# Kernel optimization log

Hardware: AMD Instinct MI355X
Metric: run time of the kernel (lower is better)

Reference implementation:

```python
import jax, jax.numpy as jnp
import numpy as np

B_, L_, DM = 8, 1024, 256
DS, DC, EX = 16, 4, 2
DI = EX * DM            # d_inner = 512
DTR = max(1, DM // 16)  # dt_rank = 16


def setup_inputs() -> dict:
    key = jax.random.key(0)
    ks = iter(jax.random.split(key, 40))
    def n(shape, s=0.02):
        return jax.random.normal(next(ks), shape, jnp.float32) * s
    inp = {"x": jax.random.normal(next(ks), (B_, L_, DM), jnp.float32)}
    inp["norm_g"] = jnp.ones((DM,), jnp.float32)
    inp["norm_b"] = jnp.zeros((DM,), jnp.float32)
    for m in ("f", "b"):
        inp[f"inW_{m}"] = n((DM, 2 * DI))
        inp[f"convW_{m}"] = n((DI, DC))
        inp[f"convB_{m}"] = jnp.zeros((DI,), jnp.float32)
        inp[f"xW_{m}"] = n((DI, DTR + 2 * DS))
        inp[f"dtW_{m}"] = n((DTR, DI))
        inp[f"dtB_{m}"] = jnp.zeros((DI,), jnp.float32)
        # ALog init: log of [1..dState] repeated over dInner rows
        inp[f"ALog_{m}"] = jnp.log(jnp.tile(jnp.arange(1, DS + 1, dtype=jnp.float32), (DI, 1)))
        inp[f"Dp_{m}"] = jnp.ones((DI,), jnp.float32)
        inp[f"outW_{m}"] = n((DI, DM))
    inp["fusW"] = n((2 * DM, DM))
    inp["fusB"] = jnp.zeros((DM,), jnp.float32)
    return inp


def _dw_conv(x, w, b):
    # causal depthwise conv1d: x [B,L,DI], w [DI,DC] -> [B,L,DI]
    xc = jnp.transpose(x, (0, 2, 1))  # B,DI,L
    out = jax.lax.conv_general_dilated(
        xc, w[:, None, :], window_strides=(1,), padding=[(DC - 1, 0)],
        dimension_numbers=("NCH", "OIH", "NCH"), feature_group_count=DI)
    return jnp.transpose(out + b[:, None], (0, 2, 1))


def _ssm(x, xW, dtW, dtB, ALog, Dp):
    # x: [B,L,DI]
    A = -jnp.exp(ALog)                                   # [DI,DS]
    xdbl = x @ xW                                        # [B,L,DTR+2*DS]
    dlt, Bp, Cp = jnp.split(xdbl, [DTR, DTR + DS], axis=-1)
    delta = jax.nn.softplus(dlt @ dtW + dtB)             # [B,L,DI]
    dA = jnp.exp(delta[..., None] * A)                   # [B,L,DI,DS]
    dBx = (delta * x)[..., None] * Bp[:, :, None, :]     # [B,L,DI,DS]

    def step(h, t):
        a, bb, c = t
        h = a * h + bb                                   # [B,DI,DS]
        y = jnp.einsum('bdn,bn->bd', h, c)
        return h, y

    h0 = jnp.zeros((x.shape[0], DI, DS), x.dtype)
    _, ys = jax.lax.scan(step, h0, (jnp.moveaxis(dA, 1, 0),
                                    jnp.moveaxis(dBx, 1, 0),
                                    jnp.moveaxis(Cp, 1, 0)))
    return jnp.moveaxis(ys, 0, 1) + Dp * x               # [B,L,DI]


def _mamba(x, inW, convW, convB, xW, dtW, dtB, ALog, Dp, outW):
    xr = x @ inW                                         # [B,L,2*DI]
    xs, res = jnp.split(xr, 2, axis=-1)
    xs = jax.nn.silu(_dw_conv(xs, convW, convB))
    y = _ssm(xs, xW, dtW, dtB, ALog, Dp)
    return (y * jax.nn.silu(res)) @ outW                 # [B,L,DM]


def reference(x, norm_g, norm_b,
              inW_f, convW_f, convB_f, xW_f, dtW_f, dtB_f, ALog_f, Dp_f, outW_f,
              inW_b, convW_b, convB_b, xW_b, dtW_b, dtB_b, ALog_b, Dp_b, outW_b,
              fusW, fusB):
    # LayerNorm
    mu = x.mean(-1, keepdims=True)
    var = ((x - mu) ** 2).mean(-1, keepdims=True)
    xn = (x - mu) * jax.lax.rsqrt(var + 1e-5) * norm_g + norm_b
    # forward-direction Mamba
    xf = _mamba(xn, inW_f, convW_f, convB_f, xW_f, dtW_f, dtB_f, ALog_f, Dp_f, outW_f)
    # backward-direction Mamba (flip along time)
    xb = _mamba(jnp.flip(xn, 1), inW_b, convW_b, convB_b, xW_b, dtW_b, dtB_b, ALog_b, Dp_b, outW_b)
    xb = jnp.flip(xb, 1)
    fused = jnp.concatenate([xf, xb], axis=-1) @ fusW + fusB
    return x + fused  # dropout is identity in eval
```

## Files before the change

kernel.cpp:

```cpp
#include <hip/hip_runtime.h>
#include <cmath>

typedef __bf16 bf16x8 __attribute__((ext_vector_type(8)));
typedef __bf16 bf16x4 __attribute__((ext_vector_type(4)));
typedef float  f32x4  __attribute__((ext_vector_type(4)));
typedef float  f32x2  __attribute__((ext_vector_type(2)));

#define B_  8
#define L_  1024
#define DM  256
#define DI  512
#define DS  16
#define DTR 16
#define M_  (B_*L_)
#define NC  32
#define CT  32
#define CC  64
#define CTC 16

__device__ inline float softplus_f(float z){
  return (z > 20.f) ? z : __logf(1.f + __expf(z));
}
__device__ inline float silu_f(float z){
  return z / (1.f + __expf(-z));
}

__device__ inline int flag_from_x(const void* x){
  const unsigned short* u = (const unsigned short*)x;
  int lane = threadIdx.x & 63;
  unsigned short v = u[2*lane];
  int e = (v >> 7) & 0xFF;
  unsigned long long m = __ballot(e >= 160 || e < 96);
  return __popcll(m) > 16;
}

struct PrepJob { const void* src; void* dst; int rows; int cols; int f32out; };
struct PrepArgs { PrepJob j[26]; int nj; };
struct TJob { const void* src; __bf16* dst; int R; int C; };
struct TArgs { TJob j[3]; int ntiles[3]; int nj; int ntot; };

__global__ __launch_bounds__(256) void wprep_k(TArgs ta, PrepArgs a, const void* xsrc){
  const int f = flag_from_x(xsrc);
  const int tid = threadIdx.x;
  if ((int)blockIdx.x < ta.ntot){
    __shared__ float tile[64][65];
    int bid = blockIdx.x;
    int jj = 0;
    while (jj < ta.nj-1 && bid >= ta.ntiles[jj]) { bid -= ta.ntiles[jj]; jj++; }
    const TJob J = ta.j[jj];
    const int tpr = J.C >> 6;
    const int tr = bid / tpr, tc = bid - tr*tpr;
    const int r0 = tr*64, c0 = tc*64;
    #pragma unroll
    for (int i=0;i<16;i++){
      int idx = i*256 + tid;
      int r = idx >> 6, c = idx & 63;
      long off = (long)(r0+r)*J.C + c0 + c;
      tile[r][c] = f ? ((const float*)J.src)[off] : (float)((const __bf16*)J.src)[off];
    }
    __syncthreads();
    #pragma unroll
    for (int i=0;i<16;i++){
      int idx = i*256 + tid;
      int c = idx >> 6, r = idx & 63;
      J.dst[(long)(c0+c)*J.R + r0 + r] = (__bf16)tile[r][c];
    }
  } else {
    int e = (blockIdx.x - ta.ntot)*256 + tid;
    #pragma unroll 1
    for (int jj=0; jj<a.nj; jj++){
      int sz = a.j[jj].rows * a.j[jj].cols;
      if (e < sz){
        int cols = a.j[jj].cols;
        int r = e / cols, c = e - r*cols;
        float v = f ? ((const float*)a.j[jj].src)[e] : (float)((const __bf16*)a.j[jj].src)[e];
        if (a.j[jj].f32out) ((float*)a.j[jj].dst)[c*a.j[jj].rows + r] = v;
        else ((__bf16*)a.j[jj].dst)[(long)c*a.j[jj].rows + r] = (__bf16)v;
        return;
      }
      e -= sz;
    }
  }
}

__global__ __launch_bounds__(256) void lnw_k(
    const void* x, const __bf16* g, const __bf16* bb, __bf16* xn,
    const __bf16* fusWt, const __bf16* outWr0, const __bf16* outWr1,
    __bf16* BtC0, __bf16* BtC1)
{
  const int bx = blockIdx.x;
  const int tid = threadIdx.x;
  const int lane = tid & 63;
  const int wid = tid >> 6;

  if (bx < M_/4){
    const int f = flag_from_x(x);
    long row = (long)bx*4 + wid;
    long base = row*DM + lane*4;
    float v0,v1,v2,v3;
    if (f){ f32x4 xv = *(const f32x4*)((const float*)x + base);
            v0=xv[0]; v1=xv[1]; v2=xv[2]; v3=xv[3]; }
    else  { bf16x4 xv = *(const bf16x4*)((const __bf16*)x + base);
            v0=(float)xv[0]; v1=(float)xv[1]; v2=(float)xv[2]; v3=(float)xv[3]; }
    float s = v0+v1+v2+v3;
    float q = v0*v0+v1*v1+v2*v2+v3*v3;
    #pragma unroll
    for (int off=32; off>0; off>>=1){ s += __shfl_xor(s,off); q += __shfl_xor(q,off); }
    float mu = s*(1.f/DM), var = q*(1.f/DM)-mu*mu;
    float rs = rsqrtf(var+1e-5f);
    bf16x4 gv = *(const bf16x4*)(g + lane*4);
    bf16x4 bv = *(const bf16x4*)(bb + lane*4);
    bf16x4 o;
    o[0]=(__bf16)((v0-mu)*rs*(float)gv[0]+(float)bv[0]);
    o[1]=(__bf16)((v1-mu)*rs*(float)gv[1]+(float)bv[1]);
    o[2]=(__bf16)((v2-mu)*rs*(float)gv[2]+(float)bv[2]);
    o[3]=(__bf16)((v3-mu)*rs*(float)gv[3]+(float)bv[3]);
    *(bf16x4*)(xn + base) = o;
  } else {
    int b2 = bx - M_/4;
    int wz  = b2 >> 5;
    int rem = b2 & 31;
    int gx = rem & 3, gy = rem >> 2;
    const __bf16* A  = fusWt + wz*DM;
    const __bf16* Bt = wz ? outWr1 : outWr0;
    __bf16* C = wz ? BtC1 : BtC0;
    const int mBase = (gx*4 + wid)*16;
    const int nBase = gy*64;
    const int lm = lane & 15;
    const int kq = (lane >> 4)*8;
    long aoff = (long)(mBase+lm)*(2*DM) + kq;
    long boff[4];
    #pragma unroll
    for (int j=0;j<4;j++) boff[j] = (long)(nBase+j*16+lm)*DM + kq;
    f32x4 acc[4] = {};
    #pragma unroll
    for (int k0=0;k0<DM;k0+=32){
      bf16x8 af = *(const bf16x8*)(A + aoff + k0);
      bf16x8 bfr[4];
      #pragma unroll
      for (int j=0;j<4;j++) bfr[j] = *(const bf16x8*)(Bt + boff[j] + k0);
      #pragma unroll
      for (int j=0;j<4;j++)
        acc[j] = __builtin_amdgcn_mfma_f32_16x16x32_bf16(af, bfr[j], acc[j], 0,0,0);
    }
    #pragma unroll
    for (int rr=0;rr<4;rr++){
      int r = mBase + (lane>>4)*4 + rr;
      #pragma unroll
      for (int j=0;j<4;j++){
        int c = nBase + j*16 + lm;
        C[(long)r*DI + c] = (__bf16)acc[j][rr];
      }
    }
  }
}

template<int BM,int BN,int KK>
__global__ __launch_bounds__(256) void gemm_in_k(
    const __bf16* A, const __bf16* B0, const __bf16* B1,
    __bf16* xz0, __bf16* xz1, __bf16* res0, __bf16* res1,
    int lda, int ldb)
{
  constexpr int TM = BM/2, TN = BN/2;
  constexpr int WMT = TM/16, WNT = TN/16;
  constexpr int LA = BM/64, LB = BN/64;

  const int dir = blockIdx.z;
  const __bf16* Bt = dir ? B1 : B0;
  __bf16* xz  = dir ? xz1 : xz0;
  __bf16* res = dir ? res1 : res0;
  const int tid  = threadIdx.x;
  const int lane = tid & 63;
  const int wid  = tid >> 6;
  const int wm = wid & 1;
  const int wn = wid >> 1;
  const int mBase = blockIdx.x * BM;
  const int nBase = blockIdx.y * BN;
  const int lm = lane & 15;
  const int kq = (lane >> 4) * 8;

  __shared__ __bf16 As[BM*32];
  __shared__ __bf16 Bs[BN*32];

  const __bf16* aS[LA];
  const __bf16* bS[LB];
  {
    int colk = (tid & 3) * 8;
    #pragma unroll
    for (int ld=0; ld<LA; ld++){
      int r = mBase + ld*64 + (tid >> 2);
      if (dir==1){ int b = r >> 10, t = r & (L_-1); r = (b<<10) + (L_-1-t); }
      aS[ld] = A + (long)r*lda + colk;
    }
    #pragma unroll
    for (int ld=0; ld<LB; ld++){
      int r = nBase + ld*64 + (tid >> 2);
      bS[ld] = Bt + (long)r*ldb + colk;
    }
  }

  f32x4 acc[WMT][WNT] = {};
  for (int k0=0; k0<KK; k0+=32){
    #pragma unroll
    for (int ld=0; ld<LA; ld++)
      __builtin_amdgcn_global_load_lds(
        (const __attribute__((address_space(1))) void*)(aS[ld] + k0),
        (__attribute__((address_space(3))) void*)(&As[ld*2048 + tid*8]), 16, 0, 0);
    #pragma unroll
    for (int ld=0; ld<LB; ld++)
      __builtin_amdgcn_global_load_lds(
        (const __attribute__((address_space(1))) void*)(bS[ld] + k0),
        (__attribute__((address_space(3))) void*)(&Bs[ld*2048 + tid*8]), 16, 0, 0);
    __syncthreads();
    bf16x8 af[WMT], bfr[WNT];
    #pragma unroll
    for (int i=0;i<WMT;i++) af[i]  = *(const bf16x8*)&As[(wm*TM + i*16 + lm)*32 + kq];
    #pragma unroll
    for (int j=0;j<WNT;j++) bfr[j] = *(const bf16x8*)&Bs[(wn*TN + j*16 + lm)*32 + kq];
    #pragma unroll
    for (int i=0;i<WMT;i++)
      #pragma unroll
      for (int j=0;j<WNT;j++)
        acc[i][j] = __builtin_amdgcn_mfma_f32_16x16x32_bf16(af[i], bfr[j], acc[i][j], 0,0,0);
    __syncthreads();
  }

  #pragma unroll
  for (int i=0;i<WMT;i++){
    #pragma unroll
    for (int rr=0;rr<4;rr++){
      int r = mBase + wm*TM + i*16 + (lane>>4)*4 + rr;
      #pragma unroll
      for (int j=0;j<WNT;j++){
        int c = nBase + wn*TN + j*16 + lm;
        float v = acc[i][j][rr];
        if (c < DI) xz[(long)r*DI + c] = (__bf16)v;
        else        res[(long)r*DI + (c-DI)] = (__bf16)v;
      }
    }
  }
}

template<int BM,int BN,int KK>
__global__ __launch_bounds__(256) void gemm_fin_k(
    const __bf16* Af, const __bf16* Ab,
    const __bf16* Bt0, const __bf16* Bt1,
    void* Cout, const __bf16* bias, const void* resid)
{
  constexpr int TM = BM/2, TN = BN/2;
  constexpr int WMT = TM/16, WNT = TN/16;
  constexpr int LA = BM/64, LB = BN/64;

  const int of = flag_from_x(resid);
  const int tid  = threadIdx.x;
  const int lane = tid & 63;
  const int wid  = tid >> 6;
  const int wm = wid & 1;
  const int wn = wid >> 1;
  const int mBase = blockIdx.x * BM;
  const int nBase = blockIdx.y * BN;
  const int lm = lane & 15;
  const int kq = (lane >> 4) * 8;

  __shared__ __bf16 As[BM*32];
  __shared__ __bf16 Bs[BN*32];

  f32x4 acc[WMT][WNT] = {};
  #pragma unroll 1
  for (int dd=0; dd<2; dd++){
    const __bf16* A  = dd ? Ab  : Af;
    const __bf16* Bt = dd ? Bt1 : Bt0;
    const __bf16* aS[LA];
    const __bf16* bS[LB];
    {
      int colk = (tid & 3) * 8;
      #pragma unroll
      for (int ld=0; ld<LA; ld++){
        int r = mBase + ld*64 + (tid >> 2);
        if (dd==1){ int b = r >> 10, t = r & (L_-1); r = (b<<10) + (L_-1-t); }
        aS[ld] = A + (long)r*DI + colk;
      }
      #pragma unroll
      for (int ld=0; ld<LB; ld++){
        int r = nBase + ld*64 + (tid >> 2);
        bS[ld] = Bt + (long)r*DI + colk;
      }
    }
    for (int k0=0; k0<KK; k0+=32){
      #pragma unroll
      for (int ld=0; ld<LA; ld++)
        __builtin_amdgcn_global_load_lds(
          (const __attribute__((address_space(1))) void*)(aS[ld] + k0),
          (__attribute__((address_space(3))) void*)(&As[ld*2048 + tid*8]), 16, 0, 0);
      #pragma unroll
      for (int ld=0; ld<LB; ld++)
        __builtin_amdgcn_global_load_lds(
          (const __attribute__((address_space(1))) void*)(bS[ld] + k0),
          (__attribute__((address_space(3))) void*)(&Bs[ld*2048 + tid*8]), 16, 0, 0);
      __syncthreads();
      bf16x8 af[WMT], bfr[WNT];
      #pragma unroll
      for (int i=0;i<WMT;i++) af[i]  = *(const bf16x8*)&As[(wm*TM + i*16 + lm)*32 + kq];
      #pragma unroll
      for (int j=0;j<WNT;j++) bfr[j] = *(const bf16x8*)&Bs[(wn*TN + j*16 + lm)*32 + kq];
      #pragma unroll
      for (int i=0;i<WMT;i++)
        #pragma unroll
        for (int j=0;j<WNT;j++)
          acc[i][j] = __builtin_amdgcn_mfma_f32_16x16x32_bf16(af[i], bfr[j], acc[i][j], 0,0,0);
      __syncthreads();
    }
  }

  #pragma unroll
  for (int i=0;i<WMT;i++){
    #pragma unroll
    for (int rr=0;rr<4;rr++){
      int r = mBase + wm*TM + i*16 + (lane>>4)*4 + rr;
      #pragma unroll
      for (int j=0;j<WNT;j++){
        int c = nBase + wn*TN + j*16 + lm;
        float v = acc[i][j][rr];
        float rsd = of ? ((const float*)resid)[(long)r*DM + c]
                       : (float)((const __bf16*)resid)[(long)r*DM + c];
        v += (float)bias[c] + rsd;
        if (of) ((float*)Cout)[(long)r*DM + c] = v;
        else    ((__bf16*)Cout)[(long)r*DM + c] = (__bf16)v;
      }
    }
  }
}

__global__ __launch_bounds__(512) void scanA_k(
    const __bf16* xz0, const __bf16* xz1,
    const float* cw0, const float* cw1,
    const __bf16* cb0, const __bf16* cb1,
    const __bf16* xW0, const __bf16* xW1,
    const float* dw0, const float* dw1,
    const __bf16* dtB0, const __bf16* dtB1,
    const float* ALf0, const float* ALf1,
    __bf16* xg0, __bf16* xg1,
    float* sg0, float* sg1,
    float* hend16, float* hend32, float* sumd16, float* sumd32)
{
  const int dir = blockIdx.z;
  const __bf16* xz  = dir ? xz1 : xz0;
  const float*  cw  = dir ? cw1 : cw0;
  const __bf16* cb  = dir ? cb1 : cb0;
  const __bf16* xWt = dir ? xW1 : xW0;
  const float*  dw  = dir ? dw1 : dw0;
  const __bf16* dtB = dir ? dtB1 : dtB0;
  const float*  ALf = dir ? ALf1 : ALf0;
  __bf16*       xg  = dir ? xg1 : xg0;
  float*        sg  = dir ? sg1 : sg0;

  const int b   = blockIdx.y;
  const int c   = blockIdx.x;
  const int tid = threadIdx.x;
  const int lane = tid & 63;
  const int wid  = tid >> 6;
  const int d   = tid;
  const int db  = dir*8 + b;
  const long row0 = (long)b*L_ + (long)c*CT;

  __shared__ __bf16 xs_s[CT*DI];
  __shared__ float  sX[CT][48];

  {
    const float q0 = cw[0*DI+d], q1 = cw[1*DI+d], q2 = cw[2*DI+d], q3 = cw[3*DI+d];
    const float cbv = (float)cb[d];
    int gt0 = c*CT;
    float xm3 = (gt0-3 >= 0) ? (float)xz[(row0-3)*DI + d] : 0.f;
    float xm2 = (gt0-2 >= 0) ? (float)xz[(row0-2)*DI + d] : 0.f;
    float xm1 = (gt0-1 >= 0) ? (float)xz[(row0-1)*DI + d] : 0.f;
    #pragma unroll 8
    for (int t=0;t<CT;t++){
      float xt = (float)xz[(row0+t)*DI + d];
      float a = cbv;
      a += xm3*q0; a += xm2*q1; a += xm1*q2; a += xt*q3;
      __bf16 sv = (__bf16)silu_f(a);
      *(__bf16*)((char*)xs_s + t*1024 + ((2*d) ^ ((t&7)<<4))) = sv;
      xg[(row0+t)*DI + d] = sv;
      xm3 = xm2; xm2 = xm1; xm1 = xt;
    }
  }
  __syncthreads();

  if (wid < 6){
    const int mb = (wid & 1) * 16;
    const int nb = (wid >> 1) * 16;
    const int lm = lane & 15;
    const int kq = (lane >> 4) * 8;
    const int row = mb + lm;
    const char* abase = (const char*)xs_s + row*1024;
    const int rsw = (row&7)<<4;
    const __bf16* Bt = xWt + (long)(nb + lm)*DI + kq;
    f32x4 acc = {};
    #pragma unroll
    for (int k0=0;k0<DI;k0+=32){
      bf16x8 af  = *(const bf16x8*)(abase + (((kq + k0)*2) ^ rsw));
      bf16x8 bfr = *(const bf16x8*)(Bt + k0);
      acc = __builtin_amdgcn_mfma_f32_16x16x32_bf16(af, bfr, acc, 0,0,0);
    }
    #pragma unroll
    for (int rr=0;rr<4;rr++){
      int r = mb + (lane>>4)*4 + rr;
      sX[r][nb + lm] = acc[rr];
      sg[(row0 + r)*48 + nb + lm] = acc[rr];
    }
  }

  f32x2 dw2[8];
  { const f32x4* p = (const f32x4*)(dw + d*DTR);
    #pragma unroll
    for (int q=0;q<4;q++){ f32x4 v=p[q];
      dw2[q*2]   = f32x2{v[0],v[1]};
      dw2[q*2+1] = f32x2{v[2],v[3]}; } }
  bool pow_ok = true;
  #pragma unroll 1
  for (int n=0;n<16;n++){
    float An = -__expf(ALf[d*DS + n]);
    pow_ok = pow_ok && (fabsf(An + (float)(n+1)) < 0.003f*(n+1));
  }
  const float dtbv = (float)dtB[d];

  f32x2 h2[8];
  #pragma unroll
  for (int i=0;i<8;i++) h2[i] = f32x2{0.f,0.f};
  float sdelta = 0.f;
  __syncthreads();

  auto scan16 = [&](int t0){
    if (pow_ok){
      #pragma unroll 2
      for (int t=t0;t<t0+16;t++){
        f32x2 z2 = f32x2{dtbv, 0.f};
        #pragma unroll
        for (int i=0;i<8;i++){
          f32x2 qv = *(const f32x2*)&sX[t][i*2];
          z2 += qv*dw2[i];
        }
        float delta = softplus_f(z2[0]+z2[1]);
        sdelta += delta;
        float xv = (float)*(const __bf16*)((const char*)xs_s + t*1024 + ((2*d) ^ ((t&7)<<4)));
        float dx = delta*xv;
        f32x2 dx2 = f32x2{dx, dx};
        float e1 = __expf(-delta), e2v = e1*e1;
        f32x2 e22 = f32x2{e2v, e2v};
        f32x2 pw = f32x2{e1, e2v};
        #pragma unroll
        for (int i=0;i<8;i++){
          f32x2 Bv = *(const f32x2*)&sX[t][16+i*2];
          h2[i] = pw*h2[i] + dx2*Bv;
          pw = pw*e22;
        }
      }
    } else {
      #pragma unroll 2
      for (int t=t0;t<t0+16;t++){
        f32x2 z2 = f32x2{dtbv, 0.f};
        #pragma unroll
        for (int i=0;i<8;i++){
          f32x2 qv = *(const f32x2*)&sX[t][i*2];
          z2 += qv*dw2[i];
        }
        float delta = softplus_f(z2[0]+z2[1]);
        sdelta += delta;
        float xv = (float)*(const __bf16*)((const char*)xs_s + t*1024 + ((2*d) ^ ((t&7)<<4)));
        float dx = delta*xv;
        #pragma unroll
        for (int i=0;i<8;i++){
          f32x2 A2 = f32x2{-__expf(ALf[d*DS+i*2]), -__expf(ALf[d*DS+i*2+1])};
          f32x2 Bv = *(const f32x2*)&sX[t][16+i*2];
          f32x2 pw = f32x2{__expf(delta*A2[0]), __expf(delta*A2[1])};
          h2[i] = pw*h2[i] + f32x2{dx,dx}*Bv;
        }
      }
    }
  };
  auto dump = [&](float* hd, float* sd){
    long hb = (((long)db*NC + c)*DI + d)*16;
    f32x4* hp = (f32x4*)(hd + hb);
    #pragma unroll
    for (int q=0;q<4;q++){
      f32x4 v; v[0]=h2[q*2][0]; v[1]=h2[q*2][1]; v[2]=h2[q*2+1][0]; v[3]=h2[q*2+1][1];
      hp[q]=v;
    }
    sd[((long)db*NC + c)*DI + d] = sdelta;
  };

  scan16(0);
  dump(hend16, sumd16);
  scan16(16);
  dump(hend32, sumd32);
}

__global__ __launch_bounds__(256) void scanB_k(
    const float* ALf0, const float* ALf1,
    const float* hend16, const float* hend32,
    const float* sumd16, const float* sumd32, float* Hbuf)
{
  int gid = blockIdx.x*256 + threadIdx.x;
  int n  = gid & 15;
  int d  = (gid>>4) & 511;
  int db = gid >> 13;
  const float* ALf = (db>=8) ? ALf1 : ALf0;
  float A_dn = -__expf(ALf[d*DS + n]);
  const long cstr  = (long)DI*16;
  const long hb = (long)db*NC*cstr + (long)d*16 + n;
  const long sb = (long)db*NC*DI + d;
  const long ob = (long)db*CC*cstr + (long)d*16 + n;
  float H = 0.f;
  #pragma unroll 1
  for (int gq=0; gq<NC/8; gq++){
    float h16[8], h32[8], e16[8], e32[8];
    #pragma unroll
    for (int k=0;k<8;k++){
      int g = gq*8+k;
      h16[k] = hend16[hb + (long)g*cstr];
      h32[k] = hend32[hb + (long)g*cstr];
      e16[k] = __expf(A_dn * sumd16[sb + (long)g*DI]);
      e32[k] = __expf(A_dn * sumd32[sb + (long)g*DI]);
    }
    #pragma unroll
    for (int k=0;k<8;k++){
      int g = gq*8+k;
      Hbuf[ob + (long)(2*g)*cstr]   = H;
      Hbuf[ob + (long)(2*g+1)*cstr] = h16[k] + e16[k]*H;
      H = h32[k] + e32[k]*H;
    }
  }
}

__global__ __launch_bounds__(512, 8) void scanC_k(
    const __bf16* __restrict__ xg0, const __bf16* __restrict__ xg1,
    const float* __restrict__ sg0, const float* __restrict__ sg1,
    __bf16* __restrict__ res0, __bf16* __restrict__ res1,
    const float* __restrict__ dw0, const float* __restrict__ dw1,
    const __bf16* __restrict__ dtB0, const __bf16* __restrict__ dtB1,
    const float* __restrict__ ALf0, const float* __restrict__ ALf1,
    const __bf16* __restrict__ Dp0, const __bf16* __restrict__ Dp1,
    const float* __restrict__ Hbuf)
{
  const int dir = blockIdx.z;
  const __bf16* xg  = dir ? xg1 : xg0;
  const float*  sg  = dir ? sg1 : sg0;
  __bf16*       res = dir ? res1 : res0;
  const float*  dw  = dir ? dw1 : dw0;
  const __bf16* dtB = dir ? dtB1 : dtB0;
  const float*  ALf = dir ? ALf1 : ALf0;
  const __bf16* Dp  = dir ? Dp1 : Dp0;

  const int b   = blockIdx.y;
  const int c   = blockIdx.x;
  const int tid = threadIdx.x;
  const int d   = tid;
  const int db  = dir*8 + b;
  const long row0 = (long)b*L_ + (long)c*CTC;

  __shared__ float sX[CTC][48];
  if (tid < (CTC*48)/4)
    ((f32x4*)sX)[tid] = ((const f32x4*)(sg + row0*48))[tid];

  f32x2 dw2[8];
  { const f32x4* p = (const f32x4*)(dw + d*DTR);
    #pragma unroll
    for (int q=0;q<4;q++){ f32x4 v=p[q];
      dw2[q*2]   = f32x2{v[0],v[1]};
      dw2[q*2+1] = f32x2{v[2],v[3]}; } }
  bool pow_ok = true;
  #pragma unroll 1
  for (int n=0;n<16;n++){
    float An = -__expf(ALf[d*DS + n]);
    pow_ok = pow_ok && (fabsf(An + (float)(n+1)) < 0.003f*(n+1));
  }
  const float dtbv = (float)dtB[d];
  const float Dpv  = (float)Dp[d];

  f32x2 h2[8];
  { long hb = (((long)db*CC + c)*DI + d)*16;
    const f32x4* p = (const f32x4*)(Hbuf + hb);
    #pragma unroll
    for (int q=0;q<4;q++){ f32x4 v = p[q];
      h2[q*2]   = f32x2{v[0],v[1]};
      h2[q*2+1] = f32x2{v[2],v[3]}; } }
  __syncthreads();

  if (pow_ok){
    #pragma unroll 2
    for (int t=0;t<CTC;t++){
      long row = row0 + t;
      f32x2 z2 = f32x2{dtbv, 0.f};
      #pragma unroll
      for (int i=0;i<8;i++){
        f32x2 qv = *(const f32x2*)&sX[t][i*2];
        z2 += qv*dw2[i];
      }
      float delta = softplus_f(z2[0]+z2[1]);
      float xv = (float)xg[row*DI + d];
      float dx = delta*xv;
      f32x2 dx2 = f32x2{dx, dx};
      float e1 = __expf(-delta), e2v = e1*e1;
      f32x2 e22 = f32x2{e2v, e2v};
      f32x2 pw = f32x2{e1, e2v};
      f32x2 p2 = f32x2{0.f, 0.f};
      #pragma unroll
      for (int i=0;i<8;i++){
        f32x2 Bv = *(const f32x2*)&sX[t][16+i*2];
        f32x2 Cv = *(const f32x2*)&sX[t][32+i*2];
        h2[i] = pw*h2[i] + dx2*Bv;
        p2 += h2[i]*Cv;
        pw = pw*e22;
      }
      float yv = p2[0] + p2[1] + Dpv*xv;
      float rv = (float)res[row*DI + d];
      res[row*DI + d] = (__bf16)(yv * silu_f(rv));
    }
  } else {
    #pragma unroll 2
    for (int t=0;t<CTC;t++){
      long row = row0 + t;
      f32x2 z2 = f32x2{dtbv, 0.f};
      #pragma unroll
      for (int i=0;i<8;i++){
        f32x2 qv = *(const f32x2*)&sX[t][i*2];
        z2 += qv*dw2[i];
      }
      float delta = softplus_f(z2[0]+z2[1]);
      float xv = (float)xg[row*DI + d];
      float dx = delta*xv;
      f32x2 p2 = f32x2{0.f, 0.f};
      #pragma unroll
      for (int i=0;i<8;i++){
        f32x2 A2 = f32x2{-__expf(ALf[d*DS+i*2]), -__expf(ALf[d*DS+i*2+1])};
        f32x2 Bv = *(const f32x2*)&sX[t][16+i*2];
        f32x2 Cv = *(const f32x2*)&sX[t][32+i*2];
        f32x2 pw = f32x2{__expf(delta*A2[0]), __expf(delta*A2[1])};
        h2[i] = pw*h2[i] + f32x2{dx,dx}*Bv;
        p2 += h2[i]*Cv;
      }
      float yv = p2[0] + p2[1] + Dpv*xv;
      float rv = (float)res[row*DI + d];
      res[row*DI + d] = (__bf16)(yv * silu_f(rv));
    }
  }
}

extern "C" void kernel_launch(void* const* d_in, const int* in_sizes, int n_in,
                              void* d_out, int out_size, void* d_ws, size_t ws_size,
                              hipStream_t stream)
{
  const size_t MB = 1u<<20;
  if (ws_size < 160*MB) return;

  char* w = (char*)d_ws;
  __bf16* xz[2]   = {(__bf16*)(w + 0),      (__bf16*)(w + 8*MB)};
  __bf16* res[2]  = {(__bf16*)(w + 16*MB),  (__bf16*)(w + 24*MB)};
  __bf16* xs_g[2] = {(__bf16*)(w + 32*MB),  (__bf16*)(w + 40*MB)};
  __bf16* xn      = (__bf16*)(w + 48*MB);

  char* wp = w + 52*MB;
  auto carve = [&](size_t bytes)->void*{
    void* p = wp;
    wp += (bytes + 255) & ~(size_t)255;
    return p;
  };
  __bf16 *inWt[2], *xWt[2], *outWr[2], *BtC[2];
  float *dtWt[2], *convWt[2];
  for (int m=0;m<2;m++){
    inWt[m]   = (__bf16*)carve((size_t)(2*DI)*DM*2);
    xWt[m]    = (__bf16*)carve((size_t)48*DI*2);
    outWr[m]  = (__bf16*)carve((size_t)DI*DM*2);
    BtC[m]    = (__bf16*)carve((size_t)DM*DI*2);
    dtWt[m]   = (float*)carve((size_t)DI*DTR*4);
    convWt[m] = (float*)carve((size_t)4*DI*4);
  }
  __bf16* fusWt = (__bf16*)carve((size_t)DM*(2*DM)*2);
  float* ALf[2] = {(float*)carve((size_t)DI*DS*4), (float*)carve((size_t)DI*DS*4)};

  char* cp = w + 57*MB;
  auto carve2 = [&](size_t elems)->__bf16*{
    __bf16* p = (__bf16*)cp;
    cp += (elems*2 + 255) & ~(size_t)255;
    return p;
  };
  __bf16* ngc = carve2(DM);
  __bf16* nbc = carve2(DM);
  __bf16 *convBc[2], *dtBc[2], *Dpc[2];
  for (int m=0;m<2;m++){
    convBc[m] = carve2(DI);
    dtBc[m]   = carve2(DI);
    Dpc[m]    = carve2(DI);
  }
  __bf16* fusBc = carve2(DM);

  float* sXg[2] = {(float*)(w + 58*MB), (float*)(w + 60*MB)};
  float* hend16 = (float*)(w + 64*MB);
  float* hend32 = (float*)(w + 80*MB);
  float* sumd16 = (float*)(w + 96*MB);
  float* sumd32 = (float*)(w + 97*MB);
  float* Hbuf   = (float*)(w + 98*MB);

  PrepArgs pa;
  int ji = 0;
  size_t tot = 0;
  auto addj = [&](const void* s, void* dst, int rows, int cols, int f32o){
    pa.j[ji++] = {s, dst, rows, cols, f32o};
    tot += (size_t)rows*cols;
  };
  for (int m=0;m<2;m++){
    int base = 3 + m*9;
    addj(d_in[base+3], xWt[m],   DI,  48,   0);
    addj(d_in[base+8], outWr[m], 1,   DI*DM,0);
    addj(d_in[base+4], dtWt[m],  DTR, DI,   1);
    addj(d_in[base+1], convWt[m],DI,  4,    1);
    addj(d_in[base+2], convBc[m],1, DI, 0);
    addj(d_in[base+5], dtBc[m],  1, DI, 0);
    addj(d_in[base+6], (void*)ALf[m], 1, DI*DS, 1);
    addj(d_in[base+7], Dpc[m],   1, DI, 0);
  }
  addj(d_in[1],  ngc, 1, DM, 0);
  addj(d_in[2],  nbc, 1, DM, 0);
  addj(d_in[22], fusBc, 1, DM, 0);
  pa.nj = ji;

  TArgs ta;
  ta.j[0] = { d_in[3],  inWt[0], DM,   2*DI }; ta.ntiles[0] = (DM/64)*((2*DI)/64);
  ta.j[1] = { d_in[12], inWt[1], DM,   2*DI }; ta.ntiles[1] = (DM/64)*((2*DI)/64);
  ta.j[2] = { d_in[21], fusWt,   2*DM, DM   }; ta.ntiles[2] = ((2*DM)/64)*(DM/64);
  ta.nj = 3;
  ta.ntot = ta.ntiles[0]+ta.ntiles[1]+ta.ntiles[2];
  int prepBlocks = (int)((tot+255)/256);
  wprep_k<<<ta.ntot + prepBlocks, 256, 0, stream>>>(ta, pa, d_in[0]);

  lnw_k<<<M_/4 + 64, 256, 0, stream>>>(
      d_in[0], ngc, nbc, xn, fusWt, outWr[0], outWr[1], BtC[0], BtC[1]);

  gemm_in_k<128,128,256><<<dim3(M_/128, (2*DI)/128, 2), 256, 0, stream>>>(
      xn, inWt[0], inWt[1], xz[0], xz[1], res[0], res[1], DM, DM);

  scanA_k<<<dim3(NC, B_, 2), 512, 0, stream>>>(
      xz[0], xz[1], convWt[0], convWt[1], convBc[0], convBc[1],
      xWt[0], xWt[1], dtWt[0], dtWt[1],
      dtBc[0], dtBc[1], ALf[0], ALf[1],
      xs_g[0], xs_g[1], sXg[0], sXg[1],
      hend16, hend32, sumd16, sumd32);
  scanB_k<<<131072/256, 256, 0, stream>>>(
      ALf[0], ALf[1], hend16, hend32, sumd16, sumd32, Hbuf);
  scanC_k<<<dim3(CC, B_, 2), 512, 0, stream>>>(
      xs_g[0], xs_g[1], sXg[0], sXg[1], res[0], res[1],
      dtWt[0], dtWt[1], dtBc[0], dtBc[1], ALf[0], ALf[1], Dpc[0], Dpc[1], Hbuf);

  gemm_fin_k<64,64,DI><<<dim3(M_/64, DM/64, 1), 256, 0, stream>>>(
      res[0], res[1], BtC[0], BtC[1], d_out, fusBc, d_in[0]);
}
```

Before: 273.2 us.

## Use 32-step chunks in scan pass C and split channels across blocks

```diff
diff --git a/kernel.cpp b/kernel.cpp
--- a/kernel.cpp
+++ b/kernel.cpp
@@ -15,8 +15,6 @@
 #define M_  (B_*L_)
 #define NC  32
 #define CT  32
-#define CC  64
-#define CTC 16
 
 __device__ inline float softplus_f(float z){
   return (z > 20.f) ? z : __logf(1.f + __expf(z));
@@ -341,7 +339,7 @@
     const float* ALf0, const float* ALf1,
     __bf16* xg0, __bf16* xg1,
     float* sg0, float* sg1,
-    float* hend16, float* hend32, float* sumd16, float* sumd32)
+    float* hend, float* sumd)
 {
   const int dir = blockIdx.z;
   const __bf16* xz  = dir ? xz1 : xz0;
@@ -376,9 +374,9 @@
     #pragma unroll 8
     for (int t=0;t<CT;t++){
       float xt = (float)xz[(row0+t)*DI + d];
-      float a = cbv;
-      a += xm3*q0; a += xm2*q1; a += xm1*q2; a += xt*q3;
-      __bf16 sv = (__bf16)silu_f(a);
+      float av = cbv;
+      av += xm3*q0; av += xm2*q1; av += xm1*q2; av += xt*q3;
+      __bf16 sv = (__bf16)silu_f(av);
       *(__bf16*)((char*)xs_s + t*1024 + ((2*d) ^ ((t&7)<<4))) = sv;
       xg[(row0+t)*DI + d] = sv;
       xm3 = xm2; xm2 = xm1; xm1 = xt;
@@ -416,12 +414,14 @@
     for (int q=0;q<4;q++){ f32x4 v=p[q];
       dw2[q*2]   = f32x2{v[0],v[1]};
       dw2[q*2+1] = f32x2{v[2],v[3]}; } }
+  float A[16];
+  { const f32x4* p = (const f32x4*)(ALf + d*DS);
+    #pragma unroll
+    for (int q=0;q<4;q++){ f32x4 v=p[q];
+      A[q*4]=-__expf(v[0]); A[q*4+1]=-__expf(v[1]); A[q*4+2]=-__expf(v[2]); A[q*4+3]=-__expf(v[3]); } }
   bool pow_ok = true;
-  #pragma unroll 1
-  for (int n=0;n<16;n++){
-    float An = -__expf(ALf[d*DS + n]);
-    pow_ok = pow_ok && (fabsf(An + (float)(n+1)) < 0.003f*(n+1));
-  }
+  #pragma unroll
+  for (int n=0;n<16;n++) pow_ok = pow_ok && (fabsf(A[n] + (float)(n+1)) < 0.003f*(n+1));
   const float dtbv = (float)dtB[d];
 
   f32x2 h2[8];
@@ -430,75 +430,65 @@
   float sdelta = 0.f;
   __syncthreads();
 
-  auto scan16 = [&](int t0){
-    if (pow_ok){
-      #pragma unroll 2
-      for (int t=t0;t<t0+16;t++){
-        f32x2 z2 = f32x2{dtbv, 0.f};
-        #pragma unroll
-        for (int i=0;i<8;i++){
-          f32x2 qv = *(const f32x2*)&sX[t][i*2];
-          z2 += qv*dw2[i];
-        }
-        float delta = softplus_f(z2[0]+z2[1]);
-        sdelta += delta;
-        float xv = (float)*(const __bf16*)((const char*)xs_s + t*1024 + ((2*d) ^ ((t&7)<<4)));
-        float dx = delta*xv;
-        f32x2 dx2 = f32x2{dx, dx};
-        float e1 = __expf(-delta), e2v = e1*e1;
-        f32x2 e22 = f32x2{e2v, e2v};
-        f32x2 pw = f32x2{e1, e2v};
-        #pragma unroll
-        for (int i=0;i<8;i++){
-          f32x2 Bv = *(const f32x2*)&sX[t][16+i*2];
-          h2[i] = pw*h2[i] + dx2*Bv;
-          pw = pw*e22;
-        }
-      }
-    } else {
-      #pragma unroll 2
-      for (int t=t0;t<t0+16;t++){
-        f32x2 z2 = f32x2{dtbv, 0.f};
-        #pragma unroll
-        for (int i=0;i<8;i++){
-          f32x2 qv = *(const f32x2*)&sX[t][i*2];
-          z2 += qv*dw2[i];
-        }
-        float delta = softplus_f(z2[0]+z2[1]);
-        sdelta += delta;
-        float xv = (float)*(const __bf16*)((const char*)xs_s + t*1024 + ((2*d) ^ ((t&7)<<4)));
-        float dx = delta*xv;
-        #pragma unroll
-        for (int i=0;i<8;i++){
-          f32x2 A2 = f32x2{-__expf(ALf[d*DS+i*2]), -__expf(ALf[d*DS+i*2+1])};
-          f32x2 Bv = *(const f32x2*)&sX[t][16+i*2];
-          f32x2 pw = f32x2{__expf(delta*A2[0]), __expf(delta*A2[1])};
-          h2[i] = pw*h2[i] + f32x2{dx,dx}*Bv;
-        }
-      }
-    }
-  };
-  auto dump = [&](float* hd, float* sd){
-    long hb = (((long)db*NC + c)*DI + d)*16;
-    f32x4* hp = (f32x4*)(hd + hb);
-    #pragma unroll
-    for (int q=0;q<4;q++){
-      f32x4 v; v[0]=h2[q*2][0]; v[1]=h2[q*2][1]; v[2]=h2[q*2+1][0]; v[3]=h2[q*2+1][1];
-      hp[q]=v;
-    }
-    sd[((long)db*NC + c)*DI + d] = sdelta;
-  };
-
-  scan16(0);
-  dump(hend16, sumd16);
-  scan16(16);
-  dump(hend32, sumd32);
+  if (pow_ok){
+    #pragma unroll 2
+    for (int t=0;t<CT;t++){
+      f32x2 z2 = f32x2{dtbv, 0.f};
+      #pragma unroll
+      for (int i=0;i<8;i++){
+        f32x2 qv = *(const f32x2*)&sX[t][i*2];
+        z2 += qv*dw2[i];
+      }
+      float delta = softplus_f(z2[0]+z2[1]);
+      sdelta += delta;
+      float xv = (float)*(const __bf16*)((const char*)xs_s + t*1024 + ((2*d) ^ ((t&7)<<4)));
+      float dx = delta*xv;
+      f32x2 dx2 = f32x2{dx, dx};
+      float e1 = __expf(-delta), e2v = e1*e1;
+      f32x2 e22 = f32x2{e2v, e2v};
+      f32x2 pw = f32x2{e1, e2v};
+      #pragma unroll
+      for (int i=0;i<8;i++){
+        f32x2 Bv = *(const f32x2*)&sX[t][16+i*2];
+        h2[i] = pw*h2[i] + dx2*Bv;
+        pw = pw*e22;
+      }
+    }
+  } else {
+    #pragma unroll 2
+    for (int t=0;t<CT;t++){
+      f32x2 z2 = f32x2{dtbv, 0.f};
+      #pragma unroll
+      for (int i=0;i<8;i++){
+        f32x2 qv = *(const f32x2*)&sX[t][i*2];
+        z2 += qv*dw2[i];
+      }
+      float delta = softplus_f(z2[0]+z2[1]);
+      sdelta += delta;
+      float xv = (float)*(const __bf16*)((const char*)xs_s + t*1024 + ((2*d) ^ ((t&7)<<4)));
+      float dx = delta*xv;
+      #pragma unroll
+      for (int i=0;i<8;i++){
+        f32x2 Bv = *(const f32x2*)&sX[t][16+i*2];
+        f32x2 pw = f32x2{__expf(delta*A[i*2]), __expf(delta*A[i*2+1])};
+        h2[i] = pw*h2[i] + f32x2{dx,dx}*Bv;
+      }
+    }
+  }
+
+  long hb = (((long)db*NC + c)*DI + d)*16;
+  f32x4* hp = (f32x4*)(hend + hb);
+  #pragma unroll
+  for (int q=0;q<4;q++){
+    f32x4 v; v[0]=h2[q*2][0]; v[1]=h2[q*2][1]; v[2]=h2[q*2+1][0]; v[3]=h2[q*2+1][1];
+    hp[q]=v;
+  }
+  sumd[((long)db*NC + c)*DI + d] = sdelta;
 }
 
 __global__ __launch_bounds__(256) void scanB_k(
     const float* ALf0, const float* ALf1,
-    const float* hend16, const float* hend32,
-    const float* sumd16, const float* sumd32, float* Hbuf)
+    const float* hend, const float* sumd, float* Hbuf)
 {
   int gid = blockIdx.x*256 + threadIdx.x;
   int n  = gid & 15;
@@ -506,33 +496,27 @@
   int db = gid >> 13;
   const float* ALf = (db>=8) ? ALf1 : ALf0;
   float A_dn = -__expf(ALf[d*DS + n]);
+  const long base0 = (((long)db*NC)*DI + d)*16 + n;
   const long cstr  = (long)DI*16;
-  const long hb = (long)db*NC*cstr + (long)d*16 + n;
-  const long sb = (long)db*NC*DI + d;
-  const long ob = (long)db*CC*cstr + (long)d*16 + n;
+  const long sbase = (long)db*NC*DI + d;
   float H = 0.f;
   #pragma unroll 1
-  for (int gq=0; gq<NC/8; gq++){
-    float h16[8], h32[8], e16[8], e32[8];
-    #pragma unroll
-    for (int k=0;k<8;k++){
-      int g = gq*8+k;
-      h16[k] = hend16[hb + (long)g*cstr];
-      h32[k] = hend32[hb + (long)g*cstr];
-      e16[k] = __expf(A_dn * sumd16[sb + (long)g*DI]);
-      e32[k] = __expf(A_dn * sumd32[sb + (long)g*DI]);
-    }
-    #pragma unroll
-    for (int k=0;k<8;k++){
-      int g = gq*8+k;
-      Hbuf[ob + (long)(2*g)*cstr]   = H;
-      Hbuf[ob + (long)(2*g+1)*cstr] = h16[k] + e16[k]*H;
-      H = h32[k] + e32[k]*H;
-    }
-  }
-}
-
-__global__ __launch_bounds__(512, 8) void scanC_k(
+  for (int g=0; g<NC/16; g++){
+    float he[16], Sv[16];
+    #pragma unroll
+    for (int k=0;k<16;k++){
+      he[k] = hend[base0 + (long)(g*16+k)*cstr];
+      Sv[k] = sumd[sbase + (long)(g*16+k)*DI];
+    }
+    #pragma unroll
+    for (int k=0;k<16;k++){
+      Hbuf[base0 + (long)(g*16+k)*cstr] = H;
+      H = he[k] + __expf(A_dn*Sv[k])*H;
+    }
+  }
+}
+
+__global__ __launch_bounds__(256, 4) void scanC_k(
     const __bf16* __restrict__ xg0, const __bf16* __restrict__ xg1,
     const float* __restrict__ sg0, const float* __restrict__ sg1,
     __bf16* __restrict__ res0, __bf16* __restrict__ res1,
@@ -542,7 +526,9 @@
     const __bf16* __restrict__ Dp0, const __bf16* __restrict__ Dp1,
     const float* __restrict__ Hbuf)
 {
-  const int dir = blockIdx.z;
+  const int zc  = blockIdx.z;
+  const int dir = zc >> 1;
+  const int dg  = zc & 1;
   const __bf16* xg  = dir ? xg1 : xg0;
   const float*  sg  = dir ? sg1 : sg0;
   __bf16*       res = dir ? res1 : res0;
@@ -553,14 +539,27 @@
 
   const int b   = blockIdx.y;
   const int c   = blockIdx.x;
-  const int tid = threadIdx.x;
-  const int d   = tid;
+  const int dl  = threadIdx.x;
+  const int d   = dg*256 + dl;
   const int db  = dir*8 + b;
-  const long row0 = (long)b*L_ + (long)c*CTC;
-
-  __shared__ float sX[CTC][48];
-  if (tid < (CTC*48)/4)
-    ((f32x4*)sX)[tid] = ((const f32x4*)(sg + row0*48))[tid];
+  const long row0 = (long)b*L_ + (long)c*CT;
+
+  __shared__ __bf16 xs_l[CT*256];
+  __shared__ float  sX[CT][48];
+
+  {
+    const __bf16* src = xg + row0*DI + dg*256;
+    #pragma unroll
+    for (int i=0;i<4;i++){
+      int r = i*8 + (dl>>5);
+      int cs = (dl&31)*8;
+      __builtin_amdgcn_global_load_lds(
+        (const __attribute__((address_space(1))) void*)(src + (long)r*DI + cs),
+        (__attribute__((address_space(3))) void*)(&xs_l[i*2048 + dl*8]), 16, 0, 0);
+    }
+  }
+  for (int v=dl; v<CT*12; v+=256)
+    ((f32x4*)sX)[v] = ((const f32x4*)(sg + row0*48))[v];
 
   f32x2 dw2[8];
   { const f32x4* p = (const f32x4*)(dw + d*DTR);
@@ -568,17 +567,19 @@
     for (int q=0;q<4;q++){ f32x4 v=p[q];
       dw2[q*2]   = f32x2{v[0],v[1]};
       dw2[q*2+1] = f32x2{v[2],v[3]}; } }
+  float A[16];
+  { const f32x4* p = (const f32x4*)(ALf + d*DS);
+    #pragma unroll
+    for (int q=0;q<4;q++){ f32x4 v=p[q];
+      A[q*4]=-__expf(v[0]); A[q*4+1]=-__expf(v[1]); A[q*4+2]=-__expf(v[2]); A[q*4+3]=-__expf(v[3]); } }
   bool pow_ok = true;
-  #pragma unroll 1
-  for (int n=0;n<16;n++){
-    float An = -__expf(ALf[d*DS + n]);
-    pow_ok = pow_ok && (fabsf(An + (float)(n+1)) < 0.003f*(n+1));
-  }
+  #pragma unroll
+  for (int n=0;n<16;n++) pow_ok = pow_ok && (fabsf(A[n] + (float)(n+1)) < 0.003f*(n+1));
   const float dtbv = (float)dtB[d];
   const float Dpv  = (float)Dp[d];
 
   f32x2 h2[8];
-  { long hb = (((long)db*CC + c)*DI + d)*16;
+  { long hb = (((long)db*NC + c)*DI + d)*16;
     const f32x4* p = (const f32x4*)(Hbuf + hb);
     #pragma unroll
     for (int q=0;q<4;q++){ f32x4 v = p[q];
@@ -588,7 +589,7 @@
 
   if (pow_ok){
     #pragma unroll 2
-    for (int t=0;t<CTC;t++){
+    for (int t=0;t<CT;t++){
       long row = row0 + t;
       f32x2 z2 = f32x2{dtbv, 0.f};
       #pragma unroll
@@ -597,7 +598,7 @@
         z2 += qv*dw2[i];
       }
       float delta = softplus_f(z2[0]+z2[1]);
-      float xv = (float)xg[row*DI + d];
+      float xv = (float)xs_l[t*256 + dl];
       float dx = delta*xv;
       f32x2 dx2 = f32x2{dx, dx};
       float e1 = __expf(-delta), e2v = e1*e1;
@@ -618,7 +619,7 @@
     }
   } else {
     #pragma unroll 2
-    for (int t=0;t<CTC;t++){
+    for (int t=0;t<CT;t++){
       long row = row0 + t;
       f32x2 z2 = f32x2{dtbv, 0.f};
       #pragma unroll
@@ -627,15 +628,14 @@
         z2 += qv*dw2[i];
       }
       float delta = softplus_f(z2[0]+z2[1]);
-      float xv = (float)xg[row*DI + d];
+      float xv = (float)xs_l[t*256 + dl];
       float dx = delta*xv;
       f32x2 p2 = f32x2{0.f, 0.f};
       #pragma unroll
       for (int i=0;i<8;i++){
-        f32x2 A2 = f32x2{-__expf(ALf[d*DS+i*2]), -__expf(ALf[d*DS+i*2+1])};
         f32x2 Bv = *(const f32x2*)&sX[t][16+i*2];
         f32x2 Cv = *(const f32x2*)&sX[t][32+i*2];
-        f32x2 pw = f32x2{__expf(delta*A2[0]), __expf(delta*A2[1])};
+        f32x2 pw = f32x2{__expf(delta*A[i*2]), __expf(delta*A[i*2+1])};
         h2[i] = pw*h2[i] + f32x2{dx,dx}*Bv;
         p2 += h2[i]*Cv;
       }
@@ -695,11 +695,9 @@
   __bf16* fusBc = carve2(DM);
 
   float* sXg[2] = {(float*)(w + 58*MB), (float*)(w + 60*MB)};
-  float* hend16 = (float*)(w + 64*MB);
-  float* hend32 = (float*)(w + 80*MB);
-  float* sumd16 = (float*)(w + 96*MB);
-  float* sumd32 = (float*)(w + 97*MB);
-  float* Hbuf   = (float*)(w + 98*MB);
+  float* hend = (float*)(w + 90*MB);
+  float* Hbuf = (float*)(w + 110*MB);
+  float* sumd = (float*)(w + 130*MB);
 
   PrepArgs pa;
   int ji = 0;
@@ -744,10 +742,9 @@
       xWt[0], xWt[1], dtWt[0], dtWt[1],
       dtBc[0], dtBc[1], ALf[0], ALf[1],
       xs_g[0], xs_g[1], sXg[0], sXg[1],
-      hend16, hend32, sumd16, sumd32);
-  scanB_k<<<131072/256, 256, 0, stream>>>(
-      ALf[0], ALf[1], hend16, hend32, sumd16, sumd32, Hbuf);
-  scanC_k<<<dim3(CC, B_, 2), 512, 0, stream>>>(
+      hend, sumd);
+  scanB_k<<<131072/256, 256, 0, stream>>>(ALf[0], ALf[1], hend, sumd, Hbuf);
+  scanC_k<<<dim3(NC, B_, 4), 256, 0, stream>>>(
       xs_g[0], xs_g[1], sXg[0], sXg[1], res[0], res[1],
       dtWt[0], dtWt[1], dtBc[0], dtBc[1], ALf[0], ALf[1], Dpc[0], Dpc[1], Hbuf);
 
```

Measured after the change: 234.5 us (median of 2 runs). -14.2%, faster.
